# Optimization experiments

Measured on AMD Instinct MI355X. Metric: run time of the kernel, lower is better.

The kernel has to match this reference:

```python
import jax, jax.numpy as jnp
import numpy as np

N_NODES = 100000
N_EDGES = 1600000
IN_DIM = 128
HID = 128
NUM_LAYERS = 10
NUM_CLASSES = 2
NUM_GRAPHS = 64


def setup_inputs() -> dict:
    key = jax.random.key(0)
    ks = jax.random.split(key, 16)
    x = jax.random.normal(ks[0], (N_NODES, IN_DIM), dtype=jnp.float32)
    # edges with no self loops (GIN_Conv calls remove_self_loops)
    src = jax.random.randint(ks[1], (N_EDGES,), 0, N_NODES)
    off = jax.random.randint(ks[2], (N_EDGES,), 1, N_NODES)
    dst = (src + off) % N_NODES
    edge_index = jnp.stack([src, dst]).astype(jnp.int64)
    batch = jnp.sort(jax.random.randint(ks[3], (N_NODES,), 0, NUM_GRAPHS)).astype(jnp.int64)
    s = 1.0 / np.sqrt(HID)
    eps = jnp.zeros((NUM_LAYERS,), dtype=jnp.float32)
    W1 = jax.random.normal(ks[4], (NUM_LAYERS, IN_DIM, HID), dtype=jnp.float32) * s
    b1 = jnp.zeros((NUM_LAYERS, HID), dtype=jnp.float32)
    W2 = jax.random.normal(ks[5], (NUM_LAYERS, HID, HID), dtype=jnp.float32) * s
    b2 = jnp.zeros((NUM_LAYERS, HID), dtype=jnp.float32)
    Wc1 = jax.random.normal(ks[6], (HID, HID), dtype=jnp.float32) * s
    bc1 = jnp.zeros((HID,), dtype=jnp.float32)
    Wc2 = jax.random.normal(ks[7], (HID, NUM_CLASSES), dtype=jnp.float32) * s
    bc2 = jnp.zeros((NUM_CLASSES,), dtype=jnp.float32)
    return {"x": x, "edge_index": edge_index, "batch": batch, "eps": eps,
            "W1": W1, "b1": b1, "W2": W2, "b2": b2,
            "Wc1": Wc1, "bc1": bc1, "Wc2": Wc2, "bc2": bc2}


def _gin_block(x, src, dst, eps_i, W1_i, b1_i, W2_i, b2_i, mlp_residual):
    # gather-scatter add aggregation: aggr[v] = sum_{(u->v)} x[u]
    aggr = jax.ops.segment_sum(x[src], dst, num_segments=N_NODES)
    h = (1.0 + eps_i) * x + aggr
    out = jnp.dot(jax.nn.relu(jnp.dot(h, W1_i) + b1_i), W2_i) + b2_i
    if mlp_residual:  # MLP internal residual (layers i > 0)
        out = out + h
    out = jax.nn.relu(out)  # ResidualGNNBlock: Identity norm, relu, Identity dropout
    out = out + x  # block residual (dims match: in_dim == hidden)
    return out


def reference(x, edge_index, batch, eps, W1, b1, W2, b2, Wc1, bc1, Wc2, bc2):
    src, dst = edge_index[0], edge_index[1]
    for i in range(NUM_LAYERS):
        x = _gin_block(x, src, dst, eps[i], W1[i], b1[i], W2[i], b2[i], mlp_residual=(i > 0))
    # global_mean_pool
    sums = jax.ops.segment_sum(x, batch, num_segments=NUM_GRAPHS)
    cnts = jax.ops.segment_sum(jnp.ones((x.shape[0], 1), x.dtype), batch, num_segments=NUM_GRAPHS)
    pooled = sums / jnp.maximum(cnts, 1.0)
    # classifier MLP (dropout inactive in eval)
    logits = jnp.dot(jax.nn.relu(jnp.dot(pooled, Wc1) + bc1), Wc2) + bc2
    return logits
```

## Files before the change

### kernel.cpp

```cpp
#include <hip/hip_runtime.h>


#define N_NODES 100000
#define N_EDGES 1600000
#define HID 128
#define NUM_LAYERS 10
#define NUM_GRAPHS 64
#define SCAN_BLOCKS ((N_NODES + 255) / 256)
#define ROWS 32
#define IDX_CAP 1024

typedef unsigned short ushort_t;

__device__ __forceinline__ float bf2f(unsigned short v) {
  return __uint_as_float(((unsigned)v) << 16);
}
__device__ __forceinline__ unsigned short f2bf(float f) {
  unsigned u = __float_as_uint(f);
  unsigned r = u + 0x7FFFu + ((u >> 16) & 1u);
  return (unsigned short)(r >> 16);
}


__global__ __launch_bounds__(256) void count_deg_kernel(const int* __restrict__ dst,
                                                        int* __restrict__ deg, int E) {
  int e = blockIdx.x * 256 + threadIdx.x;
  if (e < E) atomicAdd(&deg[dst[e]], 1);
}

__global__ __launch_bounds__(256) void block_sum_kernel(const int* __restrict__ deg,
                                                        int* __restrict__ psum, int n) {
  __shared__ int sd[256];
  int i = blockIdx.x * 256 + threadIdx.x;
  sd[threadIdx.x] = (i < n) ? deg[i] : 0;
  __syncthreads();
  for (int off = 128; off > 0; off >>= 1) {
    if (threadIdx.x < off) sd[threadIdx.x] += sd[threadIdx.x + off];
    __syncthreads();
  }
  if (threadIdx.x == 0) psum[blockIdx.x] = sd[0];
}

__global__ __launch_bounds__(512) void scan_partials_kernel(const int* __restrict__ psum,
                                                            int* __restrict__ poff, int nb) {
  __shared__ int sd[512];
  int i = threadIdx.x;
  int v = (i < nb) ? psum[i] : 0;
  sd[i] = v;
  __syncthreads();
  for (int off = 1; off < 512; off <<= 1) {
    int t = (i >= off) ? sd[i - off] : 0;
    __syncthreads();
    sd[i] += t;
    __syncthreads();
  }
  if (i < nb) poff[i] = sd[i] - v;
}

__global__ __launch_bounds__(256) void write_rs_kernel(const int* __restrict__ deg,
                                                       const int* __restrict__ poff,
                                                       int* __restrict__ rs,
                                                       int* __restrict__ cur, int n) {
  __shared__ int sd[256];
  int i = blockIdx.x * 256 + threadIdx.x;
  int v = (i < n) ? deg[i] : 0;
  sd[threadIdx.x] = v;
  __syncthreads();
  for (int off = 1; off < 256; off <<= 1) {
    int t = (threadIdx.x >= off) ? sd[threadIdx.x - off] : 0;
    __syncthreads();
    sd[threadIdx.x] += t;
    __syncthreads();
  }
  if (i < n) {
    int incl = poff[blockIdx.x] + sd[threadIdx.x];
    rs[i + 1] = incl;
    cur[i] = incl - v;
  }
  if (i == 0) rs[0] = 0;
}

__global__ __launch_bounds__(256) void fill_csr_kernel(const int* __restrict__ src,
                                                       const int* __restrict__ dst,
                                                       int* __restrict__ cur,
                                                       int* __restrict__ csr, int E) {
  int e = blockIdx.x * 256 + threadIdx.x;
  if (e < E) {
    int p = atomicAdd(&cur[dst[e]], 1);
    csr[p] = src[e];
  }
}

__global__ __launch_bounds__(256) void cast_bf16_kernel(const float* __restrict__ xin,
                                                        ushort_t* __restrict__ xh, int n4) {
  int i = blockIdx.x * 256 + threadIdx.x;
  if (i < n4) {
    float4 v = ((const float4*)xin)[i];
    ushort4 o;
    o.x = f2bf(v.x); o.y = f2bf(v.y); o.z = f2bf(v.z); o.w = f2bf(v.w);
    ((ushort4*)xh)[i] = o;
  }
}


__global__ __launch_bounds__(256, 6) void layer_kernel(const float* __restrict__ xin,
                                                       float* __restrict__ xout,
                                                       const ushort_t* __restrict__ xh_in,
                                                       ushort_t* __restrict__ xh_out,
                                                       const int* __restrict__ rs,
                                                       const int* __restrict__ csr,
                                                       const float* __restrict__ eps, int layer,
                                                       const float* __restrict__ W1,
                                                       const float* __restrict__ b1,
                                                       const float* __restrict__ W2,
                                                       const float* __restrict__ b2,
                                                       int n, int addH) {
  __shared__ float lh[ROWS * 128];
  __shared__ int lidx[IDX_CAP];
  const int tid = threadIdx.x;
  const int row0 = blockIdx.x * ROWS;
  const float4* x4 = (const float4*)xin;
  const ushort4* xh4 = (const ushort4*)xh_in;
  float4* lh4 = (float4*)lh;
  const float s = 1.0f + eps[layer];

  int rowEnd = row0 + ROWS; if (rowEnd > n) rowEnd = n;
  const int eBase = rs[row0];
  const int cnt = rs[rowEnd] - eBase;
  const int stage = (cnt < IDX_CAP) ? cnt : IDX_CAP;
  for (int t = tid; t < stage; t += 256) lidx[t] = csr[eBase + t];
  __syncthreads();

  const int w = tid >> 5;
  const int lane = tid & 31;
#pragma unroll
  for (int it = 0; it < ROWS / 8; ++it) {
    int li = it * 8 + w;
    int node = row0 + li;
    float ax = 0.f, ay = 0.f, az = 0.f, aw = 0.f;
    if (node < n) {
      float4 v = x4[node * 32 + lane];
      ax = v.x * s; ay = v.y * s; az = v.z * s; aw = v.w * s;
      const int e0 = rs[node];
      const int m = rs[node + 1] - e0;
      const int lb = e0 - eBase;
      int i = 0;
      if (lb + m <= stage) {
        for (; i + 8 <= m; i += 8) {
          int u0 = lidx[lb + i + 0], u1 = lidx[lb + i + 1];
          int u2 = lidx[lb + i + 2], u3 = lidx[lb + i + 3];
          int u4 = lidx[lb + i + 4], u5 = lidx[lb + i + 5];
          int u6 = lidx[lb + i + 6], u7 = lidx[lb + i + 7];
          ushort4 t0 = xh4[u0 * 32 + lane];
          ushort4 t1 = xh4[u1 * 32 + lane];
          ushort4 t2 = xh4[u2 * 32 + lane];
          ushort4 t3 = xh4[u3 * 32 + lane];
          ushort4 t4 = xh4[u4 * 32 + lane];
          ushort4 t5 = xh4[u5 * 32 + lane];
          ushort4 t6 = xh4[u6 * 32 + lane];
          ushort4 t7 = xh4[u7 * 32 + lane];
          ax += bf2f(t0.x) + bf2f(t1.x) + bf2f(t2.x) + bf2f(t3.x)
              + bf2f(t4.x) + bf2f(t5.x) + bf2f(t6.x) + bf2f(t7.x);
          ay += bf2f(t0.y) + bf2f(t1.y) + bf2f(t2.y) + bf2f(t3.y)
              + bf2f(t4.y) + bf2f(t5.y) + bf2f(t6.y) + bf2f(t7.y);
          az += bf2f(t0.z) + bf2f(t1.z) + bf2f(t2.z) + bf2f(t3.z)
              + bf2f(t4.z) + bf2f(t5.z) + bf2f(t6.z) + bf2f(t7.z);
          aw += bf2f(t0.w) + bf2f(t1.w) + bf2f(t2.w) + bf2f(t3.w)
              + bf2f(t4.w) + bf2f(t5.w) + bf2f(t6.w) + bf2f(t7.w);
        }
        if (i + 4 <= m) {
          int u0 = lidx[lb + i + 0], u1 = lidx[lb + i + 1];
          int u2 = lidx[lb + i + 2], u3 = lidx[lb + i + 3];
          ushort4 t0 = xh4[u0 * 32 + lane];
          ushort4 t1 = xh4[u1 * 32 + lane];
          ushort4 t2 = xh4[u2 * 32 + lane];
          ushort4 t3 = xh4[u3 * 32 + lane];
          ax += bf2f(t0.x) + bf2f(t1.x) + bf2f(t2.x) + bf2f(t3.x);
          ay += bf2f(t0.y) + bf2f(t1.y) + bf2f(t2.y) + bf2f(t3.y);
          az += bf2f(t0.z) + bf2f(t1.z) + bf2f(t2.z) + bf2f(t3.z);
          aw += bf2f(t0.w) + bf2f(t1.w) + bf2f(t2.w) + bf2f(t3.w);
          i += 4;
        }
        if (i + 2 <= m) {
          int u0 = lidx[lb + i + 0], u1 = lidx[lb + i + 1];
          ushort4 t0 = xh4[u0 * 32 + lane];
          ushort4 t1 = xh4[u1 * 32 + lane];
          ax += bf2f(t0.x) + bf2f(t1.x); ay += bf2f(t0.y) + bf2f(t1.y);
          az += bf2f(t0.z) + bf2f(t1.z); aw += bf2f(t0.w) + bf2f(t1.w);
          i += 2;
        }
        if (i < m) {
          int u = lidx[lb + i];
          ushort4 t = xh4[u * 32 + lane];
          ax += bf2f(t.x); ay += bf2f(t.y); az += bf2f(t.z); aw += bf2f(t.w);
        }
      } else {
        for (; i < m; ++i) {
          int u = csr[e0 + i];
          ushort4 t = xh4[u * 32 + lane];
          ax += bf2f(t.x); ay += bf2f(t.y); az += bf2f(t.z); aw += bf2f(t.w);
        }
      }
    }
    float4 r; r.x = ax; r.y = ay; r.z = az; r.w = aw;
    lh4[li * 32 + lane] = r;
  }
  __syncthreads();

  const int cg = tid & 31;
  const int rg = tid >> 5;
  float acc[4][4];
#pragma unroll
  for (int r = 0; r < 4; ++r) { acc[r][0] = acc[r][1] = acc[r][2] = acc[r][3] = 0.f; }

  for (int k4 = 0; k4 < 32; ++k4) {
    float4 w0 = *(const float4*)(W1 + (k4 * 4 + 0) * 128 + cg * 4);
    float4 w1 = *(const float4*)(W1 + (k4 * 4 + 1) * 128 + cg * 4);
    float4 w2 = *(const float4*)(W1 + (k4 * 4 + 2) * 128 + cg * 4);
    float4 w3 = *(const float4*)(W1 + (k4 * 4 + 3) * 128 + cg * 4);
#pragma unroll
    for (int r = 0; r < 4; ++r) {
      float4 a = *(const float4*)(lh + (rg * 4 + r) * 128 + k4 * 4);
      acc[r][0] += a.x * w0.x + a.y * w1.x + a.z * w2.x + a.w * w3.x;
      acc[r][1] += a.x * w0.y + a.y * w1.y + a.z * w2.y + a.w * w3.y;
      acc[r][2] += a.x * w0.z + a.y * w1.z + a.z * w2.z + a.w * w3.z;
      acc[r][3] += a.x * w0.w + a.y * w1.w + a.z * w2.w + a.w * w3.w;
    }
  }

  float4 hreg[4];
#pragma unroll
  for (int r = 0; r < 4; ++r) hreg[r] = *(const float4*)(lh + (rg * 4 + r) * 128 + cg * 4);
  __syncthreads();

  {
    float4 bb = *(const float4*)(b1 + cg * 4);
#pragma unroll
    for (int r = 0; r < 4; ++r) {
      float4 o;
      o.x = fmaxf(acc[r][0] + bb.x, 0.f);
      o.y = fmaxf(acc[r][1] + bb.y, 0.f);
      o.z = fmaxf(acc[r][2] + bb.z, 0.f);
      o.w = fmaxf(acc[r][3] + bb.w, 0.f);
      *(float4*)(lh + (rg * 4 + r) * 128 + cg * 4) = o;
      acc[r][0] = acc[r][1] = acc[r][2] = acc[r][3] = 0.f;
    }
  }
  __syncthreads();

  for (int k4 = 0; k4 < 32; ++k4) {
    float4 w0 = *(const float4*)(W2 + (k4 * 4 + 0) * 128 + cg * 4);
    float4 w1 = *(const float4*)(W2 + (k4 * 4 + 1) * 128 + cg * 4);
    float4 w2 = *(const float4*)(W2 + (k4 * 4 + 2) * 128 + cg * 4);
    float4 w3 = *(const float4*)(W2 + (k4 * 4 + 3) * 128 + cg * 4);
#pragma unroll
    for (int r = 0; r < 4; ++r) {
      float4 a = *(const float4*)(lh + (rg * 4 + r) * 128 + k4 * 4);
      acc[r][0] += a.x * w0.x + a.y * w1.x + a.z * w2.x + a.w * w3.x;
      acc[r][1] += a.x * w0.y + a.y * w1.y + a.z * w2.y + a.w * w3.y;
      acc[r][2] += a.x * w0.z + a.y * w1.z + a.z * w2.z + a.w * w3.z;
      acc[r][3] += a.x * w0.w + a.y * w1.w + a.z * w2.w + a.w * w3.w;
    }
  }

  float4 b2v = *(const float4*)(b2 + cg * 4);
  float4* xo4 = (float4*)xout;
  ushort4* xho4 = (ushort4*)xh_out;
#pragma unroll
  for (int r = 0; r < 4; ++r) {
    int row = row0 + rg * 4 + r;
    if (row < n) {
      float ox = acc[r][0] + b2v.x;
      float oy = acc[r][1] + b2v.y;
      float oz = acc[r][2] + b2v.z;
      float ow = acc[r][3] + b2v.w;
      if (addH) {
        ox += hreg[r].x; oy += hreg[r].y; oz += hreg[r].z; ow += hreg[r].w;
      }
      ox = fmaxf(ox, 0.f); oy = fmaxf(oy, 0.f); oz = fmaxf(oz, 0.f); ow = fmaxf(ow, 0.f);
      float4 xv = x4[row * 32 + cg];
      float4 o;
      o.x = ox + xv.x; o.y = oy + xv.y; o.z = oz + xv.z; o.w = ow + xv.w;
      xo4[row * 32 + cg] = o;
      ushort4 ob;
      ob.x = f2bf(o.x); ob.y = f2bf(o.y); ob.z = f2bf(o.z); ob.w = f2bf(o.w);
      xho4[row * 32 + cg] = ob;
    }
  }
}


__global__ __launch_bounds__(128) void pool_kernel(const float* __restrict__ x,
                                                   const int* __restrict__ batch,
                                                   float* __restrict__ pool,
                                                   int* __restrict__ gcnt, int n) {
  const int CH = 512;
  int c = threadIdx.x;
  int n0 = blockIdx.x * CH;
  if (n0 >= n) return;
  int n1 = n0 + CH; if (n1 > n) n1 = n;
  float acc = 0.f;
  int g = batch[n0];
  int cl = 0;
  for (int i = n0; i < n1; ++i) {
    int gi = batch[i];
    if (gi != g) {
      atomicAdd(&pool[g * 128 + c], acc);
      if (c == 0) atomicAdd(&gcnt[g], cl);
      acc = 0.f; cl = 0; g = gi;
    }
    acc += x[i * 128 + c];
    cl++;
  }
  atomicAdd(&pool[g * 128 + c], acc);
  if (c == 0) atomicAdd(&gcnt[g], cl);
}


__global__ __launch_bounds__(128) void classifier_kernel(const float* __restrict__ pool,
                                                         const int* __restrict__ gcnt,
                                                         const float* __restrict__ Wc1,
                                                         const float* __restrict__ bc1,
                                                         const float* __restrict__ Wc2,
                                                         const float* __restrict__ bc2,
                                                         float* __restrict__ out) {
  __shared__ float prow[128];
  __shared__ float hid[128];
  int g = blockIdx.x;
  int c = threadIdx.x;
  float cf = (float)gcnt[g];
  if (cf < 1.f) cf = 1.f;
  prow[c] = pool[g * 128 + c] / cf;
  __syncthreads();
  float a = bc1[c];
  for (int k = 0; k < 128; ++k) a += prow[k] * Wc1[k * 128 + c];
  hid[c] = fmaxf(a, 0.f);
  __syncthreads();
  if (c < 2) {
    float a2 = bc2[c];
    for (int k = 0; k < 128; ++k) a2 += hid[k] * Wc2[k * 2 + c];
    out[g * 2 + c] = a2;
  }
}


extern "C" void kernel_launch(void* const* d_in, const int* in_sizes, int n_in,
                              void* d_out, int out_size, void* d_ws, size_t ws_size,
                              hipStream_t stream) {
  const float* x_in = (const float*)d_in[0];
  const int* edge_index = (const int*)d_in[1];
  const int* batch = (const int*)d_in[2];
  const float* eps = (const float*)d_in[3];
  const float* W1 = (const float*)d_in[4];
  const float* b1 = (const float*)d_in[5];
  const float* W2 = (const float*)d_in[6];
  const float* b2 = (const float*)d_in[7];
  const float* Wc1 = (const float*)d_in[8];
  const float* bc1 = (const float*)d_in[9];
  const float* Wc2 = (const float*)d_in[10];
  const float* bc2 = (const float*)d_in[11];
  float* out = (float*)d_out;

  const int N = N_NODES, E = N_EDGES;
  const int* src = edge_index;
  const int* dst = edge_index + E;

  float* xa = (float*)d_ws;
  ushort_t* xha = (ushort_t*)(xa + (size_t)N * 128);
  ushort_t* xhb = xha + (size_t)N * 128;
  int* deg = (int*)(xhb + (size_t)N * 128);
  int* rs = deg + N;
  int* cur = rs + (N + 1);
  int* csr = cur + N;
  float* pool = (float*)(csr + E);
  int* gcnt = (int*)(pool + NUM_GRAPHS * 128);
  int* psum = gcnt + NUM_GRAPHS;
  int* poff = psum + SCAN_BLOCKS;

  hipMemsetAsync(deg, 0, N * sizeof(int), stream);

  count_deg_kernel<<<(E + 255) / 256, 256, 0, stream>>>(dst, deg, E);
  block_sum_kernel<<<SCAN_BLOCKS, 256, 0, stream>>>(deg, psum, N);
  scan_partials_kernel<<<1, 512, 0, stream>>>(psum, poff, SCAN_BLOCKS);
  write_rs_kernel<<<SCAN_BLOCKS, 256, 0, stream>>>(deg, poff, rs, cur, N);
  fill_csr_kernel<<<(E + 255) / 256, 256, 0, stream>>>(src, dst, cur, csr, E);

  cast_bf16_kernel<<<(N * 32 + 255) / 256, 256, 0, stream>>>(x_in, xha, N * 32);

  const int NB = (N + ROWS - 1) / ROWS;
  for (int i = 0; i < NUM_LAYERS; ++i) {
    const float* xi = (i == 0) ? x_in : xa;
    const ushort_t* gin = (i % 2 == 0) ? xha : xhb;
    ushort_t* gout = (i % 2 == 0) ? xhb : xha;
    layer_kernel<<<NB, 256, 0, stream>>>(xi, xa, gin, gout, rs, csr, eps, i,
                                         W1 + (size_t)i * 128 * 128, b1 + (size_t)i * 128,
                                         W2 + (size_t)i * 128 * 128, b2 + (size_t)i * 128,
                                         N, i > 0 ? 1 : 0);
  }

  hipMemsetAsync(pool, 0, NUM_GRAPHS * 128 * sizeof(float), stream);
  hipMemsetAsync(gcnt, 0, NUM_GRAPHS * sizeof(int), stream);
  pool_kernel<<<(N + 511) / 512, 128, 0, stream>>>(xa, batch, pool, gcnt, N);
  classifier_kernel<<<NUM_GRAPHS, 128, 0, stream>>>(pool, gcnt, Wc1, bc1, Wc2, bc2, out);
}
```

Baseline: 2.301 ms.

## Warp-specialize persistent layer kernel to overlap neighbor gather with MLP

The layer kernel becomes persistent: a fixed grid of 768 blocks loops over 32-row tiles. Half the threads (producers) gather and aggregate neighbor rows for the next tile into a double-buffered shared tile, while the other half (consumers) run both 128x128 MLP matmuls on the current tile. Neighbor indices are now read straight from the CSR and broadcast with lane shuffles, 16 at a time, which replaces the per-block shared-memory index staging. This is meant to hide the latency of the irregular gather behind the matmul work, at the cost of fewer threads issuing gathers, more shared memory, and a lower occupancy target.

After: 2.506 ms. 8.9% more time.

```diff
diff --git a/kernel.cpp b/kernel.cpp
--- a/kernel.cpp
+++ b/kernel.cpp
@@ -8,7 +8,8 @@
 #define NUM_GRAPHS 64
 #define SCAN_BLOCKS ((N_NODES + 255) / 256)
 #define ROWS 32
-#define IDX_CAP 1024
+#define NT (N_NODES / ROWS)
+#define GRID 768
 
 typedef unsigned short ushort_t;
 
@@ -102,8 +103,106 @@
   }
 }
 
-
-__global__ __launch_bounds__(256, 6) void layer_kernel(const float* __restrict__ xin,
+__device__ __forceinline__ float4 gather_row(const float4* __restrict__ x4,
+                                             const ushort4* __restrict__ xh4,
+                                             const int* __restrict__ rs,
+                                             const int* __restrict__ csr,
+                                             int node, int lane, float s) {
+  float4 v = x4[node * 32 + lane];
+  float ax = v.x * s, ay = v.y * s, az = v.z * s, aw = v.w * s;
+  const int e0 = rs[node];
+  const int m = rs[node + 1] - e0;
+  int i = 0;
+  while (i + 16 <= m) {
+    int myi = csr[e0 + i + (lane & 15)];
+    int u0 = __shfl(myi, 0, 32),  u1 = __shfl(myi, 1, 32);
+    int u2 = __shfl(myi, 2, 32),  u3 = __shfl(myi, 3, 32);
+    int u4 = __shfl(myi, 4, 32),  u5 = __shfl(myi, 5, 32);
+    int u6 = __shfl(myi, 6, 32),  u7 = __shfl(myi, 7, 32);
+    int u8 = __shfl(myi, 8, 32),  u9 = __shfl(myi, 9, 32);
+    int u10 = __shfl(myi, 10, 32), u11 = __shfl(myi, 11, 32);
+    int u12 = __shfl(myi, 12, 32), u13 = __shfl(myi, 13, 32);
+    int u14 = __shfl(myi, 14, 32), u15 = __shfl(myi, 15, 32);
+    ushort4 t0 = xh4[u0 * 32 + lane],  t1 = xh4[u1 * 32 + lane];
+    ushort4 t2 = xh4[u2 * 32 + lane],  t3 = xh4[u3 * 32 + lane];
+    ushort4 t4 = xh4[u4 * 32 + lane],  t5 = xh4[u5 * 32 + lane];
+    ushort4 t6 = xh4[u6 * 32 + lane],  t7 = xh4[u7 * 32 + lane];
+    ushort4 t8 = xh4[u8 * 32 + lane],  t9 = xh4[u9 * 32 + lane];
+    ushort4 t10 = xh4[u10 * 32 + lane], t11 = xh4[u11 * 32 + lane];
+    ushort4 t12 = xh4[u12 * 32 + lane], t13 = xh4[u13 * 32 + lane];
+    ushort4 t14 = xh4[u14 * 32 + lane], t15 = xh4[u15 * 32 + lane];
+    ax += bf2f(t0.x) + bf2f(t1.x) + bf2f(t2.x) + bf2f(t3.x)
+        + bf2f(t4.x) + bf2f(t5.x) + bf2f(t6.x) + bf2f(t7.x)
+        + bf2f(t8.x) + bf2f(t9.x) + bf2f(t10.x) + bf2f(t11.x)
+        + bf2f(t12.x) + bf2f(t13.x) + bf2f(t14.x) + bf2f(t15.x);
+    ay += bf2f(t0.y) + bf2f(t1.y) + bf2f(t2.y) + bf2f(t3.y)
+        + bf2f(t4.y) + bf2f(t5.y) + bf2f(t6.y) + bf2f(t7.y)
+        + bf2f(t8.y) + bf2f(t9.y) + bf2f(t10.y) + bf2f(t11.y)
+        + bf2f(t12.y) + bf2f(t13.y) + bf2f(t14.y) + bf2f(t15.y);
+    az += bf2f(t0.z) + bf2f(t1.z) + bf2f(t2.z) + bf2f(t3.z)
+        + bf2f(t4.z) + bf2f(t5.z) + bf2f(t6.z) + bf2f(t7.z)
+        + bf2f(t8.z) + bf2f(t9.z) + bf2f(t10.z) + bf2f(t11.z)
+        + bf2f(t12.z) + bf2f(t13.z) + bf2f(t14.z) + bf2f(t15.z);
+    aw += bf2f(t0.w) + bf2f(t1.w) + bf2f(t2.w) + bf2f(t3.w)
+        + bf2f(t4.w) + bf2f(t5.w) + bf2f(t6.w) + bf2f(t7.w)
+        + bf2f(t8.w) + bf2f(t9.w) + bf2f(t10.w) + bf2f(t11.w)
+        + bf2f(t12.w) + bf2f(t13.w) + bf2f(t14.w) + bf2f(t15.w);
+    i += 16;
+  }
+  int c = m - i;
+  if (c) {
+    int sl = (lane & 15);
+    int myi = csr[e0 + i + (sl < c ? sl : 0)];
+    int b = 0;
+    if (c & 8) {
+      int u0 = __shfl(myi, b + 0, 32), u1 = __shfl(myi, b + 1, 32);
+      int u2 = __shfl(myi, b + 2, 32), u3 = __shfl(myi, b + 3, 32);
+      int u4 = __shfl(myi, b + 4, 32), u5 = __shfl(myi, b + 5, 32);
+      int u6 = __shfl(myi, b + 6, 32), u7 = __shfl(myi, b + 7, 32);
+      ushort4 t0 = xh4[u0 * 32 + lane], t1 = xh4[u1 * 32 + lane];
+      ushort4 t2 = xh4[u2 * 32 + lane], t3 = xh4[u3 * 32 + lane];
+      ushort4 t4 = xh4[u4 * 32 + lane], t5 = xh4[u5 * 32 + lane];
+      ushort4 t6 = xh4[u6 * 32 + lane], t7 = xh4[u7 * 32 + lane];
+      ax += bf2f(t0.x) + bf2f(t1.x) + bf2f(t2.x) + bf2f(t3.x)
+          + bf2f(t4.x) + bf2f(t5.x) + bf2f(t6.x) + bf2f(t7.x);
+      ay += bf2f(t0.y) + bf2f(t1.y) + bf2f(t2.y) + bf2f(t3.y)
+          + bf2f(t4.y) + bf2f(t5.y) + bf2f(t6.y) + bf2f(t7.y);
+      az += bf2f(t0.z) + bf2f(t1.z) + bf2f(t2.z) + bf2f(t3.z)
+          + bf2f(t4.z) + bf2f(t5.z) + bf2f(t6.z) + bf2f(t7.z);
+      aw += bf2f(t0.w) + bf2f(t1.w) + bf2f(t2.w) + bf2f(t3.w)
+          + bf2f(t4.w) + bf2f(t5.w) + bf2f(t6.w) + bf2f(t7.w);
+      b += 8;
+    }
+    if (c & 4) {
+      int u0 = __shfl(myi, b + 0, 32), u1 = __shfl(myi, b + 1, 32);
+      int u2 = __shfl(myi, b + 2, 32), u3 = __shfl(myi, b + 3, 32);
+      ushort4 t0 = xh4[u0 * 32 + lane], t1 = xh4[u1 * 32 + lane];
+      ushort4 t2 = xh4[u2 * 32 + lane], t3 = xh4[u3 * 32 + lane];
+      ax += bf2f(t0.x) + bf2f(t1.x) + bf2f(t2.x) + bf2f(t3.x);
+      ay += bf2f(t0.y) + bf2f(t1.y) + bf2f(t2.y) + bf2f(t3.y);
+      az += bf2f(t0.z) + bf2f(t1.z) + bf2f(t2.z) + bf2f(t3.z);
+      aw += bf2f(t0.w) + bf2f(t1.w) + bf2f(t2.w) + bf2f(t3.w);
+      b += 4;
+    }
+    if (c & 2) {
+      int u0 = __shfl(myi, b + 0, 32), u1 = __shfl(myi, b + 1, 32);
+      ushort4 t0 = xh4[u0 * 32 + lane], t1 = xh4[u1 * 32 + lane];
+      ax += bf2f(t0.x) + bf2f(t1.x); ay += bf2f(t0.y) + bf2f(t1.y);
+      az += bf2f(t0.z) + bf2f(t1.z); aw += bf2f(t0.w) + bf2f(t1.w);
+      b += 2;
+    }
+    if (c & 1) {
+      int u0 = __shfl(myi, b, 32);
+      ushort4 t0 = xh4[u0 * 32 + lane];
+      ax += bf2f(t0.x); ay += bf2f(t0.y); az += bf2f(t0.z); aw += bf2f(t0.w);
+    }
+  }
+  float4 r; r.x = ax; r.y = ay; r.z = az; r.w = aw;
+  return r;
+}
+
+
+__global__ __launch_bounds__(256, 3) void layer_kernel(const float* __restrict__ xin,
                                                        float* __restrict__ xout,
                                                        const ushort_t* __restrict__ xh_in,
                                                        ushort_t* __restrict__ xh_out,
@@ -115,177 +214,149 @@
                                                        const float* __restrict__ W2,
                                                        const float* __restrict__ b2,
                                                        int n, int addH) {
-  __shared__ float lh[ROWS * 128];
-  __shared__ int lidx[IDX_CAP];
+  __shared__ float lh[2][ROWS * 128];
+  __shared__ float lmid[ROWS * 128];
   const int tid = threadIdx.x;
-  const int row0 = blockIdx.x * ROWS;
+  const int bid = blockIdx.x;
   const float4* x4 = (const float4*)xin;
   const ushort4* xh4 = (const ushort4*)xh_in;
-  float4* lh4 = (float4*)lh;
   const float s = 1.0f + eps[layer];
 
-  int rowEnd = row0 + ROWS; if (rowEnd > n) rowEnd = n;
-  const int eBase = rs[row0];
-  const int cnt = rs[rowEnd] - eBase;
-  const int stage = (cnt < IDX_CAP) ? cnt : IDX_CAP;
-  for (int t = tid; t < stage; t += 256) lidx[t] = csr[eBase + t];
-  __syncthreads();
-
-  const int w = tid >> 5;
+  int ntiles = 0;
+  for (int t = bid; t < NT; t += GRID) ntiles++;
+
+  const bool producer = (tid < 128);
+  const int g = (tid >> 5) & 3;
   const int lane = tid & 31;
-#pragma unroll
-  for (int it = 0; it < ROWS / 8; ++it) {
-    int li = it * 8 + w;
-    int node = row0 + li;
-    float ax = 0.f, ay = 0.f, az = 0.f, aw = 0.f;
-    if (node < n) {
-      float4 v = x4[node * 32 + lane];
-      ax = v.x * s; ay = v.y * s; az = v.z * s; aw = v.w * s;
-      const int e0 = rs[node];
-      const int m = rs[node + 1] - e0;
-      const int lb = e0 - eBase;
-      int i = 0;
-      if (lb + m <= stage) {
-        for (; i + 8 <= m; i += 8) {
-          int u0 = lidx[lb + i + 0], u1 = lidx[lb + i + 1];
-          int u2 = lidx[lb + i + 2], u3 = lidx[lb + i + 3];
-          int u4 = lidx[lb + i + 4], u5 = lidx[lb + i + 5];
-          int u6 = lidx[lb + i + 6], u7 = lidx[lb + i + 7];
-          ushort4 t0 = xh4[u0 * 32 + lane];
-          ushort4 t1 = xh4[u1 * 32 + lane];
-          ushort4 t2 = xh4[u2 * 32 + lane];
-          ushort4 t3 = xh4[u3 * 32 + lane];
-          ushort4 t4 = xh4[u4 * 32 + lane];
-          ushort4 t5 = xh4[u5 * 32 + lane];
-          ushort4 t6 = xh4[u6 * 32 + lane];
-          ushort4 t7 = xh4[u7 * 32 + lane];
-          ax += bf2f(t0.x) + bf2f(t1.x) + bf2f(t2.x) + bf2f(t3.x)
-              + bf2f(t4.x) + bf2f(t5.x) + bf2f(t6.x) + bf2f(t7.x);
-          ay += bf2f(t0.y) + bf2f(t1.y) + bf2f(t2.y) + bf2f(t3.y)
-              + bf2f(t4.y) + bf2f(t5.y) + bf2f(t6.y) + bf2f(t7.y);
-          az += bf2f(t0.z) + bf2f(t1.z) + bf2f(t2.z) + bf2f(t3.z)
-              + bf2f(t4.z) + bf2f(t5.z) + bf2f(t6.z) + bf2f(t7.z);
-          aw += bf2f(t0.w) + bf2f(t1.w) + bf2f(t2.w) + bf2f(t3.w)
-              + bf2f(t4.w) + bf2f(t5.w) + bf2f(t6.w) + bf2f(t7.w);
+  const int ctid = tid - 128;
+  const int cg = ctid & 31;
+  const int rg = ctid >> 5;
+
+  if (producer && ntiles > 0) {
+    int row0 = (bid)*ROWS;
+#pragma unroll
+    for (int rr = 0; rr < 8; ++rr) {
+      int li = g + rr * 4;
+      int node = row0 + li;
+      if (node < n) {
+        float4 h = gather_row(x4, xh4, rs, csr, node, lane, s);
+        *(float4*)(&lh[0][li * 128 + lane * 4]) = h;
+      }
+    }
+  }
+  __syncthreads();
+
+  for (int k = 0; k < ntiles; ++k) {
+    const int tcur = bid + k * GRID;
+    const int tnext = tcur + GRID;
+    const int slot = k & 1;
+    const int nslot = slot ^ 1;
+    const int row0 = tcur * ROWS;
+
+    if (producer) {
+      if (k + 1 < ntiles) {
+        int nrow0 = tnext * ROWS;
+#pragma unroll
+        for (int rr = 0; rr < 4; ++rr) {
+          int li = g + rr * 4;
+          int node = nrow0 + li;
+          if (node < n) {
+            float4 h = gather_row(x4, xh4, rs, csr, node, lane, s);
+            *(float4*)(&lh[nslot][li * 128 + lane * 4]) = h;
+          }
         }
-        if (i + 4 <= m) {
-          int u0 = lidx[lb + i + 0], u1 = lidx[lb + i + 1];
-          int u2 = lidx[lb + i + 2], u3 = lidx[lb + i + 3];
-          ushort4 t0 = xh4[u0 * 32 + lane];
-          ushort4 t1 = xh4[u1 * 32 + lane];
-          ushort4 t2 = xh4[u2 * 32 + lane];
-          ushort4 t3 = xh4[u3 * 32 + lane];
-          ax += bf2f(t0.x) + bf2f(t1.x) + bf2f(t2.x) + bf2f(t3.x);
-          ay += bf2f(t0.y) + bf2f(t1.y) + bf2f(t2.y) + bf2f(t3.y);
-          az += bf2f(t0.z) + bf2f(t1.z) + bf2f(t2.z) + bf2f(t3.z);
-          aw += bf2f(t0.w) + bf2f(t1.w) + bf2f(t2.w) + bf2f(t3.w);
-          i += 4;
+      }
+    } else {
+      float acc[8][4];
+#pragma unroll
+      for (int r = 0; r < 8; ++r) { acc[r][0] = acc[r][1] = acc[r][2] = acc[r][3] = 0.f; }
+      const float* lhs = lh[slot];
+      for (int k4 = 0; k4 < 32; ++k4) {
+        float4 w0 = *(const float4*)(W1 + (k4 * 4 + 0) * 128 + cg * 4);
+        float4 w1 = *(const float4*)(W1 + (k4 * 4 + 1) * 128 + cg * 4);
+        float4 w2 = *(const float4*)(W1 + (k4 * 4 + 2) * 128 + cg * 4);
+        float4 w3 = *(const float4*)(W1 + (k4 * 4 + 3) * 128 + cg * 4);
+#pragma unroll
+        for (int r = 0; r < 8; ++r) {
+          float4 a = *(const float4*)(lhs + (rg * 8 + r) * 128 + k4 * 4);
+          acc[r][0] += a.x * w0.x + a.y * w1.x + a.z * w2.x + a.w * w3.x;
+          acc[r][1] += a.x * w0.y + a.y * w1.y + a.z * w2.y + a.w * w3.y;
+          acc[r][2] += a.x * w0.z + a.y * w1.z + a.z * w2.z + a.w * w3.z;
+          acc[r][3] += a.x * w0.w + a.y * w1.w + a.z * w2.w + a.w * w3.w;
         }
-        if (i + 2 <= m) {
-          int u0 = lidx[lb + i + 0], u1 = lidx[lb + i + 1];
-          ushort4 t0 = xh4[u0 * 32 + lane];
-          ushort4 t1 = xh4[u1 * 32 + lane];
-          ax += bf2f(t0.x) + bf2f(t1.x); ay += bf2f(t0.y) + bf2f(t1.y);
-          az += bf2f(t0.z) + bf2f(t1.z); aw += bf2f(t0.w) + bf2f(t1.w);
-          i += 2;
+      }
+      float4 bb = *(const float4*)(b1 + cg * 4);
+#pragma unroll
+      for (int r = 0; r < 8; ++r) {
+        float4 o;
+        o.x = fmaxf(acc[r][0] + bb.x, 0.f);
+        o.y = fmaxf(acc[r][1] + bb.y, 0.f);
+        o.z = fmaxf(acc[r][2] + bb.z, 0.f);
+        o.w = fmaxf(acc[r][3] + bb.w, 0.f);
+        *(float4*)(lmid + (rg * 8 + r) * 128 + cg * 4) = o;
+      }
+    }
+    __syncthreads();
+
+    if (producer) {
+      if (k + 1 < ntiles) {
+        int nrow0 = tnext * ROWS;
+#pragma unroll
+        for (int rr = 0; rr < 4; ++rr) {
+          int li = 16 + g + rr * 4;
+          int node = nrow0 + li;
+          if (node < n) {
+            float4 h = gather_row(x4, xh4, rs, csr, node, lane, s);
+            *(float4*)(&lh[nslot][li * 128 + lane * 4]) = h;
+          }
         }
-        if (i < m) {
-          int u = lidx[lb + i];
-          ushort4 t = xh4[u * 32 + lane];
-          ax += bf2f(t.x); ay += bf2f(t.y); az += bf2f(t.z); aw += bf2f(t.w);
+      }
+    } else {
+      float acc[8][4];
+#pragma unroll
+      for (int r = 0; r < 8; ++r) { acc[r][0] = acc[r][1] = acc[r][2] = acc[r][3] = 0.f; }
+      for (int k4 = 0; k4 < 32; ++k4) {
+        float4 w0 = *(const float4*)(W2 + (k4 * 4 + 0) * 128 + cg * 4);
+        float4 w1 = *(const float4*)(W2 + (k4 * 4 + 1) * 128 + cg * 4);
+        float4 w2 = *(const float4*)(W2 + (k4 * 4 + 2) * 128 + cg * 4);
+        float4 w3 = *(const float4*)(W2 + (k4 * 4 + 3) * 128 + cg * 4);
+#pragma unroll
+        for (int r = 0; r < 8; ++r) {
+          float4 a = *(const float4*)(lmid + (rg * 8 + r) * 128 + k4 * 4);
+          acc[r][0] += a.x * w0.x + a.y * w1.x + a.z * w2.x + a.w * w3.x;
+          acc[r][1] += a.x * w0.y + a.y * w1.y + a.z * w2.y + a.w * w3.y;
+          acc[r][2] += a.x * w0.z + a.y * w1.z + a.z * w2.z + a.w * w3.z;
+          acc[r][3] += a.x * w0.w + a.y * w1.w + a.z * w2.w + a.w * w3.w;
         }
-      } else {
-        for (; i < m; ++i) {
-          int u = csr[e0 + i];
-          ushort4 t = xh4[u * 32 + lane];
-          ax += bf2f(t.x); ay += bf2f(t.y); az += bf2f(t.z); aw += bf2f(t.w);
+      }
+      float4 b2v = *(const float4*)(b2 + cg * 4);
+      float4* xo4 = (float4*)xout;
+      ushort4* xho4 = (ushort4*)xh_out;
+      const float* lhs = lh[slot];
+#pragma unroll
+      for (int r = 0; r < 8; ++r) {
+        int row = row0 + rg * 8 + r;
+        if (row < n) {
+          float ox = acc[r][0] + b2v.x;
+          float oy = acc[r][1] + b2v.y;
+          float oz = acc[r][2] + b2v.z;
+          float ow = acc[r][3] + b2v.w;
+          if (addH) {
+            float4 hv = *(const float4*)(lhs + (rg * 8 + r) * 128 + cg * 4);
+            ox += hv.x; oy += hv.y; oz += hv.z; ow += hv.w;
+          }
+          ox = fmaxf(ox, 0.f); oy = fmaxf(oy, 0.f); oz = fmaxf(oz, 0.f); ow = fmaxf(ow, 0.f);
+          float4 xv = x4[row * 32 + cg];
+          float4 o;
+          o.x = ox + xv.x; o.y = oy + xv.y; o.z = oz + xv.z; o.w = ow + xv.w;
+          xo4[row * 32 + cg] = o;
+          ushort4 ob;
+          ob.x = f2bf(o.x); ob.y = f2bf(o.y); ob.z = f2bf(o.z); ob.w = f2bf(o.w);
+          xho4[row * 32 + cg] = ob;
         }
       }
     }
-    float4 r; r.x = ax; r.y = ay; r.z = az; r.w = aw;
-    lh4[li * 32 + lane] = r;
-  }
-  __syncthreads();
-
-  const int cg = tid & 31;
-  const int rg = tid >> 5;
-  float acc[4][4];
-#pragma unroll
-  for (int r = 0; r < 4; ++r) { acc[r][0] = acc[r][1] = acc[r][2] = acc[r][3] = 0.f; }
-
-  for (int k4 = 0; k4 < 32; ++k4) {
-    float4 w0 = *(const float4*)(W1 + (k4 * 4 + 0) * 128 + cg * 4);
-    float4 w1 = *(const float4*)(W1 + (k4 * 4 + 1) * 128 + cg * 4);
-    float4 w2 = *(const float4*)(W1 + (k4 * 4 + 2) * 128 + cg * 4);
-    float4 w3 = *(const float4*)(W1 + (k4 * 4 + 3) * 128 + cg * 4);
-#pragma unroll
-    for (int r = 0; r < 4; ++r) {
-      float4 a = *(const float4*)(lh + (rg * 4 + r) * 128 + k4 * 4);
-      acc[r][0] += a.x * w0.x + a.y * w1.x + a.z * w2.x + a.w * w3.x;
-      acc[r][1] += a.x * w0.y + a.y * w1.y + a.z * w2.y + a.w * w3.y;
-      acc[r][2] += a.x * w0.z + a.y * w1.z + a.z * w2.z + a.w * w3.z;
-      acc[r][3] += a.x * w0.w + a.y * w1.w + a.z * w2.w + a.w * w3.w;
-    }
-  }
-
-  float4 hreg[4];
-#pragma unroll
-  for (int r = 0; r < 4; ++r) hreg[r] = *(const float4*)(lh + (rg * 4 + r) * 128 + cg * 4);
-  __syncthreads();
-
-  {
-    float4 bb = *(const float4*)(b1 + cg * 4);
-#pragma unroll
-    for (int r = 0; r < 4; ++r) {
-      float4 o;
-      o.x = fmaxf(acc[r][0] + bb.x, 0.f);
-      o.y = fmaxf(acc[r][1] + bb.y, 0.f);
-      o.z = fmaxf(acc[r][2] + bb.z, 0.f);
-      o.w = fmaxf(acc[r][3] + bb.w, 0.f);
-      *(float4*)(lh + (rg * 4 + r) * 128 + cg * 4) = o;
-      acc[r][0] = acc[r][1] = acc[r][2] = acc[r][3] = 0.f;
-    }
-  }
-  __syncthreads();
-
-  for (int k4 = 0; k4 < 32; ++k4) {
-    float4 w0 = *(const float4*)(W2 + (k4 * 4 + 0) * 128 + cg * 4);
-    float4 w1 = *(const float4*)(W2 + (k4 * 4 + 1) * 128 + cg * 4);
-    float4 w2 = *(const float4*)(W2 + (k4 * 4 + 2) * 128 + cg * 4);
-    float4 w3 = *(const float4*)(W2 + (k4 * 4 + 3) * 128 + cg * 4);
-#pragma unroll
-    for (int r = 0; r < 4; ++r) {
-      float4 a = *(const float4*)(lh + (rg * 4 + r) * 128 + k4 * 4);
-      acc[r][0] += a.x * w0.x + a.y * w1.x + a.z * w2.x + a.w * w3.x;
-      acc[r][1] += a.x * w0.y + a.y * w1.y + a.z * w2.y + a.w * w3.y;
-      acc[r][2] += a.x * w0.z + a.y * w1.z + a.z * w2.z + a.w * w3.z;
-      acc[r][3] += a.x * w0.w + a.y * w1.w + a.z * w2.w + a.w * w3.w;
-    }
-  }
-
-  float4 b2v = *(const float4*)(b2 + cg * 4);
-  float4* xo4 = (float4*)xout;
-  ushort4* xho4 = (ushort4*)xh_out;
-#pragma unroll
-  for (int r = 0; r < 4; ++r) {
-    int row = row0 + rg * 4 + r;
-    if (row < n) {
-      float ox = acc[r][0] + b2v.x;
-      float oy = acc[r][1] + b2v.y;
-      float oz = acc[r][2] + b2v.z;
-      float ow = acc[r][3] + b2v.w;
-      if (addH) {
-        ox += hreg[r].x; oy += hreg[r].y; oz += hreg[r].z; ow += hreg[r].w;
-      }
-      ox = fmaxf(ox, 0.f); oy = fmaxf(oy, 0.f); oz = fmaxf(oz, 0.f); ow = fmaxf(ow, 0.f);
-      float4 xv = x4[row * 32 + cg];
-      float4 o;
-      o.x = ox + xv.x; o.y = oy + xv.y; o.z = oz + xv.z; o.w = ow + xv.w;
-      xo4[row * 32 + cg] = o;
-      ushort4 ob;
-      ob.x = f2bf(o.x); ob.y = f2bf(o.y); ob.z = f2bf(o.z); ob.w = f2bf(o.w);
-      xho4[row * 32 + cg] = ob;
-    }
+    __syncthreads();
   }
 }
 
@@ -387,15 +458,14 @@
 
   cast_bf16_kernel<<<(N * 32 + 255) / 256, 256, 0, stream>>>(x_in, xha, N * 32);
 
-  const int NB = (N + ROWS - 1) / ROWS;
   for (int i = 0; i < NUM_LAYERS; ++i) {
     const float* xi = (i == 0) ? x_in : xa;
     const ushort_t* gin = (i % 2 == 0) ? xha : xhb;
     ushort_t* gout = (i % 2 == 0) ? xhb : xha;
-    layer_kernel<<<NB, 256, 0, stream>>>(xi, xa, gin, gout, rs, csr, eps, i,
-                                         W1 + (size_t)i * 128 * 128, b1 + (size_t)i * 128,
-                                         W2 + (size_t)i * 128 * 128, b2 + (size_t)i * 128,
-                                         N, i > 0 ? 1 : 0);
+    layer_kernel<<<GRID, 256, 0, stream>>>(xi, xa, gin, gout, rs, csr, eps, i,
+                                           W1 + (size_t)i * 128 * 128, b1 + (size_t)i * 128,
+                                           W2 + (size_t)i * 128 * 128, b2 + (size_t)i * 128,
+                                           N, i > 0 ? 1 : 0);
   }
 
   hipMemsetAsync(pool, 0, NUM_GRAPHS * 128 * sizeof(float), stream);
```
